# Kernel tuning notes

Hardware: AMD Instinct MI355X
Metric: run time of the kernel (lower is better)

## Reference

```python
import jax, jax.numpy as jnp
import numpy as np

N, INPUTDIM, OUTDIM, GRIDSIZE = 32768, 64, 256, 32


def setup_inputs() -> dict:
    key = jax.random.key(0)
    k1, k2 = jax.random.split(key)
    x = jax.random.normal(k1, (N, INPUTDIM), dtype=jnp.float32)
    # xavier_uniform over tensor of shape (2, outdim, inputdim, gridsize):
    # fan_in = inputdim*gridsize, fan_out = outdim*gridsize (torch treats dim0=fan_out-ish,
    # but exact init scale is irrelevant for correctness; use a matching uniform range)
    fan_in = INPUTDIM * GRIDSIZE
    fan_out = OUTDIM * GRIDSIZE
    bound = float(np.sqrt(6.0 / (fan_in + fan_out)))
    fouriercoeffs = jax.random.uniform(
        k2, (2, OUTDIM, INPUTDIM, GRIDSIZE), dtype=jnp.float32,
        minval=-bound, maxval=bound)
    bias = jnp.zeros((1, OUTDIM), dtype=jnp.float32)
    return {"x": x, "fouriercoeffs": fouriercoeffs, "bias": bias}


def reference(x, fouriercoeffs, bias):
    # gridsize_param rounds back to GRIDSIZE at init -> static.
    g = fouriercoeffs.shape[-1]
    k = jnp.arange(1, g + 1, dtype=x.dtype)  # (g,)
    # Fourier feature expansion: (N, inputdim, g)
    xk = x[:, :, None] * k[None, None, :]
    c = jnp.cos(xk)
    s = jnp.sin(xk)
    # Contract over (inputdim, gridsize) -> two GEMMs over flattened dim
    y = jnp.einsum('nig,oig->no', c, fouriercoeffs[0])
    y = y + jnp.einsum('nig,oig->no', s, fouriercoeffs[1])
    y = y + bias  # (1, outdim) broadcasts over N
    return y
```

## Files before the change

### kernel.cpp

```cpp
#include <hip/hip_runtime.h>


#define IDIM 64
#define ODIM 256
#define KDIM 4096
#define BM 64

typedef __attribute__((ext_vector_type(8))) unsigned short ushort8_t;
typedef __bf16 bf16x8 __attribute__((ext_vector_type(8)));
typedef float floatx4 __attribute__((ext_vector_type(4)));

__device__ __forceinline__ unsigned short f2bf_rne(float f) {
  unsigned int u = __float_as_uint(f);
  return (unsigned short)((u + 0x7FFFu + ((u >> 16) & 1u)) >> 16);
}

__global__ void __launch_bounds__(256) wconv(const float* __restrict__ fc,
                                             unsigned short* __restrict__ Wr) {
  int t = blockIdx.x * 256 + threadIdx.x;
  int lane = t & 63;
  int j = (t >> 6) & 7;
  int bb = t >> 9;
  int wn2 = bb & 1;
  int wk = (bb >> 1) & 1;
  int kt = bb >> 2;
  int o = wn2 * 128 + j * 16 + (lane & 15);
  int g0 = (lane >> 4) * 8;
  const float* src = fc + ((size_t)wk << 19) + o * 2048 + kt * 32 + g0;
  const float4 v0 = *(const float4*)(src);
  const float4 v1 = *(const float4*)(src + 4);
  ushort8_t r;
  r[0] = f2bf_rne(v0.x);
  r[1] = f2bf_rne(v0.y);
  r[2] = f2bf_rne(v0.z);
  r[3] = f2bf_rne(v0.w);
  r[4] = f2bf_rne(v1.x);
  r[5] = f2bf_rne(v1.y);
  r[6] = f2bf_rne(v1.z);
  r[7] = f2bf_rne(v1.w);
  *(ushort8_t*)(Wr + (size_t)t * 8) = r;
}

__global__ void __launch_bounds__(256, 2) fkan_gemm(const float* __restrict__ X,
                                                    const unsigned short* __restrict__ Wr,
                                                    const float* __restrict__ bias,
                                                    float* __restrict__ out) {
  __shared__ __align__(16) unsigned char smem[66560];
  unsigned short* const AsBase = (unsigned short*)smem;
  float* const red = (float*)smem;

  const int t = threadIdx.x;
  const int wv = t >> 6;
  const int ln = t & 63;
  const int lm = ln & 15;
  const int quad = ln >> 4;
  const int wk = wv & 1;
  const int wn2 = wv >> 1;
  const int m0 = blockIdx.x * BM;

  const int arow = t >> 2;
  const int q = t & 3;
  const float g0f = (float)(8 * q + 1);

  const int ga_c = arow * 8 + (q ^ (arow & 7));
  const int ga_s = arow * 8 + ((4 + q) ^ (arow & 7));

  const unsigned short* const bwave = Wr + (size_t)(wk * 2 + wn2) * 4096 + ln * 8;

  floatx4 acc[4][8];
#pragma unroll
  for (int a = 0; a < 4; ++a)
#pragma unroll
    for (int b = 0; b < 8; ++b)
      acc[a][b] = (floatx4){0.0f, 0.0f, 0.0f, 0.0f};

  const float* xptr = X + (size_t)(m0 + arow) * IDIM;

  auto features = [&](float xv, int buf) {
    const float inv2pi = 0.15915494309189535f;
    float u = xv * inv2pi;
    float u0 = u * g0f;
    float c1 = __builtin_amdgcn_cosf(u);
    float s1 = __builtin_amdgcn_sinf(u);
    float C = __builtin_amdgcn_cosf(u0);
    float S = __builtin_amdgcn_sinf(u0);
    bf16x8 cb, sb;
    cb[0] = (__bf16)C;
    sb[0] = (__bf16)S;
#pragma unroll
    for (int jj = 1; jj < 8; ++jj) {
      float Cn = __builtin_fmaf(C, c1, -(S * s1));
      float Sn = __builtin_fmaf(S, c1, (C * s1));
      C = Cn;
      S = Sn;
      cb[jj] = (__bf16)C;
      sb[jj] = (__bf16)S;
    }
    ushort8_t* As8 = (ushort8_t*)(AsBase + buf * 4096);
    As8[ga_c] = __builtin_bit_cast(ushort8_t, cb);
    As8[ga_s] = __builtin_bit_cast(ushort8_t, sb);
  };

  bf16x8 breg[8];

  auto ktstep = [&](int ktn, int cur, int nxt) {
    float xn = xptr[ktn];
    const ushort8_t* A8 = (const ushort8_t*)(AsBase + cur * 4096);
    const int ch = wk * 4 + quad;
    bf16x8 af[4];
#pragma unroll
    for (int mt = 0; mt < 4; ++mt) {
      int r = mt * 16 + lm;
      af[mt] = __builtin_bit_cast(bf16x8, A8[r * 8 + (ch ^ (r & 7))]);
    }
    const unsigned short* bn = bwave + (size_t)ktn * 16384;

    __builtin_amdgcn_s_setprio(1);
#pragma unroll
    for (int nt = 0; nt < 8; ++nt) {
#pragma unroll
      for (int mt = 0; mt < 4; ++mt)
        acc[mt][nt] = __builtin_amdgcn_mfma_f32_16x16x32_bf16(
            af[mt], breg[nt], acc[mt][nt], 0, 0, 0);
      breg[nt] = __builtin_bit_cast(bf16x8, *(const ushort8_t*)(bn + nt * 512));
    }
    __builtin_amdgcn_s_setprio(0);

    features(xn, nxt);
    __syncthreads();
  };

  auto ktlast = [&](int cur) {
    const ushort8_t* A8 = (const ushort8_t*)(AsBase + cur * 4096);
    const int ch = wk * 4 + quad;
    bf16x8 af[4];
#pragma unroll
    for (int mt = 0; mt < 4; ++mt) {
      int r = mt * 16 + lm;
      af[mt] = __builtin_bit_cast(bf16x8, A8[r * 8 + (ch ^ (r & 7))]);
    }
    __builtin_amdgcn_s_setprio(1);
#pragma unroll
    for (int nt = 0; nt < 8; ++nt)
#pragma unroll
      for (int mt = 0; mt < 4; ++mt)
        acc[mt][nt] = __builtin_amdgcn_mfma_f32_16x16x32_bf16(
            af[mt], breg[nt], acc[mt][nt], 0, 0, 0);
    __builtin_amdgcn_s_setprio(0);
  };

#pragma unroll
  for (int nt = 0; nt < 8; ++nt)
    breg[nt] = __builtin_bit_cast(bf16x8, *(const ushort8_t*)(bwave + nt * 512));
  features(xptr[0], 0);
  __syncthreads();

  for (int kt = 0; kt < 62; kt += 2) {
    ktstep(kt + 1, 0, 1);
    ktstep(kt + 2, 1, 0);
  }
  ktstep(63, 0, 1);
  ktlast(1);

  __syncthreads();
  if (wk == 1) {
#pragma unroll
    for (int mt = 0; mt < 4; ++mt)
#pragma unroll
      for (int nt = 0; nt < 8; ++nt) {
        int col = wn2 * 128 + nt * 16 + lm;
#pragma unroll
        for (int idx = 0; idx < 4; ++idx)
          red[(mt * 16 + quad * 4 + idx) * 260 + col] = acc[mt][nt][idx];
      }
  }
  __syncthreads();
  if (wk == 0) {
#pragma unroll
    for (int nt = 0; nt < 8; ++nt) {
      int col = wn2 * 128 + nt * 16 + lm;
      float bv = bias[col];
#pragma unroll
      for (int mt = 0; mt < 4; ++mt) {
        int rbase = m0 + mt * 16 + quad * 4;
#pragma unroll
        for (int idx = 0; idx < 4; ++idx)
          out[(size_t)(rbase + idx) * ODIM + col] =
              acc[mt][nt][idx] + red[(mt * 16 + quad * 4 + idx) * 260 + col] + bv;
      }
    }
  }
}

extern "C" void kernel_launch(void* const* d_in, const int* in_sizes, int n_in,
                              void* d_out, int out_size, void* d_ws, size_t ws_size,
                              hipStream_t stream) {
  const float* x = (const float*)d_in[0];
  const float* fc = (const float*)d_in[1];
  const float* bias = (const float*)d_in[2];
  float* out = (float*)d_out;
  unsigned short* Wr = (unsigned short*)d_ws;

  hipLaunchKernelGGL(wconv, dim3(512), dim3(256), 0, stream, fc, Wr);
  hipLaunchKernelGGL(fkan_gemm, dim3(512), dim3(256), 0, stream, x, Wr, bias, out);
}
```

Measured before the change: 132.4 us.

## Batch four k-steps per LDS buffer to cut barriers by four

Each double-buffered LDS stage now holds features for four k-tiles instead of one. The block runs four MFMA clusters interleaved with feature generation before hitting a single __syncthreads. This removes three of every four block barriers in the main loop and gives more room for overlapping trig work with MFMAs. In exchange it uses four times the LDS for A buffers (32 KB, still inside the existing allocation) and makes the pipeline prologue and epilogue longer.

Result: faster. 128.3 us (-3.1%).

```diff
diff --git a/kernel.cpp b/kernel.cpp
--- a/kernel.cpp
+++ b/kernel.cpp
@@ -76,7 +76,7 @@
 
   const float* xptr = X + (size_t)(m0 + arow) * IDIM;
 
-  auto features = [&](float xv, int buf) {
+  auto features = [&](float xv, int buf, int j) {
     const float inv2pi = 0.15915494309189535f;
     float u = xv * inv2pi;
     float u0 = u * g0f;
@@ -96,16 +96,15 @@
       cb[jj] = (__bf16)C;
       sb[jj] = (__bf16)S;
     }
-    ushort8_t* As8 = (ushort8_t*)(AsBase + buf * 4096);
+    ushort8_t* As8 = (ushort8_t*)(AsBase + buf * 16384 + j * 4096);
     As8[ga_c] = __builtin_bit_cast(ushort8_t, cb);
     As8[ga_s] = __builtin_bit_cast(ushort8_t, sb);
   };
 
   bf16x8 breg[8];
 
-  auto ktstep = [&](int ktn, int cur, int nxt) {
-    float xn = xptr[ktn];
-    const ushort8_t* A8 = (const ushort8_t*)(AsBase + cur * 4096);
+  auto cluster = [&](int buf, int j, int reload_kt, bool do_reload) {
+    const ushort8_t* A8 = (const ushort8_t*)(AsBase + buf * 16384 + j * 4096);
     const int ch = wk * 4 + quad;
     bf16x8 af[4];
 #pragma unroll
@@ -113,8 +112,7 @@
       int r = mt * 16 + lm;
       af[mt] = __builtin_bit_cast(bf16x8, A8[r * 8 + (ch ^ (r & 7))]);
     }
-    const unsigned short* bn = bwave + (size_t)ktn * 16384;
-
+    const unsigned short* bn = bwave + (size_t)reload_kt * 16384;
     __builtin_amdgcn_s_setprio(1);
 #pragma unroll
     for (int nt = 0; nt < 8; ++nt) {
@@ -122,45 +120,48 @@
       for (int mt = 0; mt < 4; ++mt)
         acc[mt][nt] = __builtin_amdgcn_mfma_f32_16x16x32_bf16(
             af[mt], breg[nt], acc[mt][nt], 0, 0, 0);
-      breg[nt] = __builtin_bit_cast(bf16x8, *(const ushort8_t*)(bn + nt * 512));
+      if (do_reload)
+        breg[nt] = __builtin_bit_cast(bf16x8, *(const ushort8_t*)(bn + nt * 512));
     }
     __builtin_amdgcn_s_setprio(0);
-
-    features(xn, nxt);
+  };
+
+  auto ktquad = [&](int s, int cur, int nxt) {
+    int k0 = 4 * s;
+    float xn0 = xptr[k0 + 4];
+    float xn1 = xptr[k0 + 5];
+    float xn2 = xptr[k0 + 6];
+    float xn3 = xptr[k0 + 7];
+    cluster(cur, 0, k0 + 1, true);
+    features(xn0, nxt, 0);
+    cluster(cur, 1, k0 + 2, true);
+    features(xn1, nxt, 1);
+    cluster(cur, 2, k0 + 3, true);
+    features(xn2, nxt, 2);
+    cluster(cur, 3, k0 + 4, true);
+    features(xn3, nxt, 3);
     __syncthreads();
   };
 
-  auto ktlast = [&](int cur) {
-    const ushort8_t* A8 = (const ushort8_t*)(AsBase + cur * 4096);
-    const int ch = wk * 4 + quad;
-    bf16x8 af[4];
-#pragma unroll
-    for (int mt = 0; mt < 4; ++mt) {
-      int r = mt * 16 + lm;
-      af[mt] = __builtin_bit_cast(bf16x8, A8[r * 8 + (ch ^ (r & 7))]);
-    }
-    __builtin_amdgcn_s_setprio(1);
-#pragma unroll
-    for (int nt = 0; nt < 8; ++nt)
-#pragma unroll
-      for (int mt = 0; mt < 4; ++mt)
-        acc[mt][nt] = __builtin_amdgcn_mfma_f32_16x16x32_bf16(
-            af[mt], breg[nt], acc[mt][nt], 0, 0, 0);
-    __builtin_amdgcn_s_setprio(0);
-  };
-
 #pragma unroll
   for (int nt = 0; nt < 8; ++nt)
     breg[nt] = __builtin_bit_cast(bf16x8, *(const ushort8_t*)(bwave + nt * 512));
-  features(xptr[0], 0);
+  features(xptr[0], 0, 0);
+  features(xptr[1], 0, 1);
+  features(xptr[2], 0, 2);
+  features(xptr[3], 0, 3);
   __syncthreads();
 
-  for (int kt = 0; kt < 62; kt += 2) {
-    ktstep(kt + 1, 0, 1);
-    ktstep(kt + 2, 1, 0);
+  for (int s = 0; s < 14; s += 2) {
+    ktquad(s, 0, 1);
+    ktquad(s + 1, 1, 0);
   }
-  ktstep(63, 0, 1);
-  ktlast(1);
+  ktquad(14, 0, 1);
+
+  cluster(1, 0, 61, true);
+  cluster(1, 1, 62, true);
+  cluster(1, 2, 63, true);
+  cluster(1, 3, 0, false);
 
   __syncthreads();
   if (wk == 1) {
```
